# Optimization experiments

Measured on AMD Instinct MI355X. Metric: run time of the kernel, lower is better.

## Reference

```python
import jax, jax.numpy as jnp
import numpy as np

NUM_HEADS = 16

def setup_inputs() -> dict:
    key = jax.random.key(0)
    ks = jax.random.split(key, 5)
    b, n, d = 2, 2048, 1024
    s = 0.02
    return {
        "x": jax.random.normal(ks[0], (b, n, d), jnp.float32),
        "wq": jax.random.normal(ks[1], (d, d), jnp.float32) * s,
        "wk": jax.random.normal(ks[2], (d, d), jnp.float32) * s,
        "wv": jax.random.normal(ks[3], (d, d), jnp.float32) * s,
        "wo": jax.random.normal(ks[4], (d, d), jnp.float32) * s,
        "bo": jnp.zeros((d,), jnp.float32),
    }

def reference(x, wq, wk, wv, wo, bo):
    b, n, c = x.shape
    h = NUM_HEADS
    hd = c // h
    scale = hd ** -0.5
    # qkv projections (qkv_bias=False); torch Linear computes x @ W.T
    def split_heads(t):
        return t.reshape(b, n, h, hd).transpose(0, 2, 1, 3)  # b h n d
    q = split_heads(x @ wq.T)
    k = split_heads(x @ wk.T)
    v = split_heads(x @ wv.T)
    dots = jnp.einsum('bhid,bhjd->bhij', q, k) * scale
    attn = jax.nn.softmax(dots, axis=-1)  # attn_drop=0 -> identity
    out = jnp.einsum('bhij,bhjd->bhid', attn, v)
    out = out.transpose(0, 2, 1, 3).reshape(b, n, c)
    out = out @ wo.T + bo  # proj_drop=0 -> identity
    return out
```

## Files before the change

kernel.cpp:

```cpp
#include <hip/hip_runtime.h>
#include <hip/hip_bf16.h>

typedef float f32x4 __attribute__((ext_vector_type(4)));
typedef short short8 __attribute__((ext_vector_type(8)));
typedef short short4v __attribute__((ext_vector_type(4)));

#define MFMA(a, b, c) __builtin_amdgcn_mfma_f32_16x16x32_bf16((a), (b), (c), 0, 0, 0)

#if __has_builtin(__builtin_amdgcn_exp2f)
#define EXP2(x) __builtin_amdgcn_exp2f(x)
#else
#define EXP2(x) exp2f(x)
#endif

#define B_  2
#define N_  2048
#define C_  1024
#define H_  16
#define HD_ 64
#define M_  (B_ * N_)

#define QSCALE 0.18033688011112042f

typedef const __attribute__((address_space(1))) void* gp_t;
typedef __attribute__((address_space(3))) void* sp_t;
#define GLL16(g, s) __builtin_amdgcn_global_load_lds((gp_t)(const void*)(g), (sp_t)(void*)(s), 16, 0, 0)

__device__ __forceinline__ short f2bf(float f) {
    union { float fv; unsigned u; } v; v.fv = f;
    unsigned r = v.u + 0x7fffu + ((v.u >> 16) & 1u);
    return (short)(r >> 16);
}
__device__ __forceinline__ unsigned pack_rne(float a, float b) {
    return (unsigned)(unsigned short)f2bf(a) | ((unsigned)(unsigned short)f2bf(b) << 16);
}

__global__ __launch_bounds__(256) void convert_kernel(
    const float* __restrict__ x,  const float* __restrict__ wq,
    const float* __restrict__ wk, const float* __restrict__ wv,
    const float* __restrict__ wo, short* __restrict__ dst)
{
    size_t e = ((size_t)blockIdx.x * 256 + threadIdx.x) * 8;
    const float* src; size_t off;
    if (e < 4194304)      { src = x;  off = e; }
    else if (e < 5242880) { src = wq; off = e - 4194304; }
    else if (e < 6291456) { src = wk; off = e - 5242880; }
    else if (e < 7340032) { src = wv; off = e - 6291456; }
    else                  { src = wo; off = e - 7340032; }
    float4 a = *(const float4*)(src + off);
    float4 b = *(const float4*)(src + off + 4);
    short8 s;
    s[0] = f2bf(a.x); s[1] = f2bf(a.y); s[2] = f2bf(a.z); s[3] = f2bf(a.w);
    s[4] = f2bf(b.x); s[5] = f2bf(b.y); s[6] = f2bf(b.z); s[7] = f2bf(b.w);
    *(short8*)(dst + e) = s;
}

__global__ __launch_bounds__(256) void qkv_gemm(
    const short* __restrict__ xb, const short* __restrict__ Wb,
    short* __restrict__ Qb, short* __restrict__ Kb, short* __restrict__ Vt)
{
    const int m0 = blockIdx.x * 128;
    const int n0 = blockIdx.y * 128;
    __shared__ short As[128 * 32];
    __shared__ short Bs[128 * 32];
    const int tid  = threadIdx.x;
    const int wave = tid >> 6, lane = tid & 63;
    const int quad = lane >> 4, l16 = lane & 15;
    const int wr = (wave >> 1) * 64, wc = (wave & 1) * 64;

    f32x4 acc[4][4] = {};

    for (int kk = 0; kk < C_; kk += 32) {
        __syncthreads();
        #pragma unroll
        for (int it = 0; it < 2; ++it) {
            int f = (it * 256 + tid) * 8;
            int row = f >> 5, col = f & 31;
            GLL16(xb + (size_t)(m0 + row) * C_ + kk + col, &As[f]);
            GLL16(Wb + (size_t)(n0 + row) * C_ + kk + col, &Bs[f]);
        }
        __syncthreads();
        short8 af[4], bf[4];
        #pragma unroll
        for (int mi = 0; mi < 4; ++mi) af[mi] = *(const short8*)&As[(wr + mi * 16 + l16) * 32 + quad * 8];
        #pragma unroll
        for (int ni = 0; ni < 4; ++ni) bf[ni] = *(const short8*)&Bs[(wc + ni * 16 + l16) * 32 + quad * 8];
        #pragma unroll
        for (int mi = 0; mi < 4; ++mi)
        #pragma unroll
        for (int ni = 0; ni < 4; ++ni)
            acc[mi][ni] = MFMA(af[mi], bf[ni], acc[mi][ni]);
    }

    const int which = n0 >> 10;
    const int nb = n0 & 1023;
    #pragma unroll
    for (int mi = 0; mi < 4; ++mi)
    #pragma unroll
    for (int ni = 0; ni < 4; ++ni)
    #pragma unroll
    for (int r = 0; r < 4; ++r) {
        int m  = m0 + wr + mi * 16 + quad * 4 + r;
        int cc = nb + wc + ni * 16 + l16;
        float av = acc[mi][ni][r];
        if (which == 0) av *= QSCALE;
        short bv = f2bf(av);
        int bb = m >> 11, ns = m & (N_ - 1);
        int h = cc >> 6, d = cc & 63;
        size_t bh = (size_t)(bb * H_ + h);
        if (which == 0)      Qb[(bh * N_ + ns) * HD_ + d] = bv;
        else if (which == 1) Kb[(bh * N_ + ns) * HD_ + d] = bv;
        else                 Vt[(bh * HD_ + d) * N_ + ns] = bv;
    }
}

__global__ __launch_bounds__(256, 2) void attn_kernel(
    const short* __restrict__ Qb, const short* __restrict__ Kb,
    const short* __restrict__ Vt, short* __restrict__ Ob)
{
    const int bh = blockIdx.y;
    const int b = bh >> 4, h = bh & (H_ - 1);
    const int i0 = blockIdx.x * 128;
    __shared__ short Qs[128 * 64];
    __shared__ short Ks[2][64 * 64];
    __shared__ short Vs[2][64 * 64];
    const int tid  = threadIdx.x;
    const int wave = tid >> 6, lane = tid & 63;
    const int quad = lane >> 4, l16 = lane & 15;
    const int sw = l16 & 7;

    const short* Qg = Qb + ((size_t)bh * N_ + i0) * HD_;
    const short* Kg = Kb + (size_t)bh * N_ * HD_;
    const short* Vg = Vt + (size_t)bh * HD_ * N_;

    const int row0 = tid >> 3,  c0 = (tid & 7) ^ (row0 & 7);
    const int row1 = row0 + 32, c1 = (tid & 7) ^ (row1 & 7);
    const short* KgA0 = Kg + row0 * HD_ + c0 * 8;
    const short* KgA1 = Kg + row1 * HD_ + c1 * 8;
    const short* VgA0 = Vg + (size_t)row0 * N_ + c0 * 8;
    const short* VgA1 = Vg + (size_t)row1 * N_ + c1 * 8;

    #pragma unroll
    for (int it = 0; it < 4; ++it) {
        int s = it * 256 + tid;
        int row = s >> 3, c = (s & 7) ^ (row & 7);
        GLL16(Qg + row * HD_ + c * 8, &Qs[s * 8]);
    }
    GLL16(KgA0, &Ks[0][tid * 8]);
    GLL16(KgA1, &Ks[0][(tid + 256) * 8]);
    GLL16(VgA0, &Vs[0][tid * 8]);
    GLL16(VgA1, &Vs[0][(tid + 256) * 8]);
    __syncthreads();

    short8 qf[2][2];
    #pragma unroll
    for (int s = 0; s < 2; ++s) {
        int row = (wave * 32 + s * 16 + l16) * 64;
        qf[s][0] = *(const short8*)&Qs[row + ((quad ^ sw) * 8)];
        qf[s][1] = *(const short8*)&Qs[row + (((quad + 4) ^ sw) * 8)];
    }

    f32x4 o[2][4] = {};
    float lrow[2] = {0.f, 0.f};

    for (int jt = 0; jt < N_ / 64; ++jt) {
        const int cur = jt & 1;
        if (jt + 1 < N_ / 64) {
            int j1 = (jt + 1) * 64;
            GLL16(KgA0 + (size_t)j1 * HD_, &Ks[cur ^ 1][tid * 8]);
            GLL16(KgA1 + (size_t)j1 * HD_, &Ks[cur ^ 1][(tid + 256) * 8]);
            GLL16(VgA0 + j1, &Vs[cur ^ 1][tid * 8]);
            GLL16(VgA1 + j1, &Vs[cur ^ 1][(tid + 256) * 8]);
        }
        const short* Kc = Ks[cur];
        const short* Vc = Vs[cur];

        #pragma unroll
        for (int half = 0; half < 2; ++half) {
            unsigned pq[2][4];
            #pragma unroll
            for (int nio = 0; nio < 2; ++nio) {
                int ni = half * 2 + nio;
                int krow = (ni * 16 + l16) * 64;
                short8 kf0 = *(const short8*)&Kc[krow + ((quad ^ sw) * 8)];
                short8 kf1 = *(const short8*)&Kc[krow + (((quad + 4) ^ sw) * 8)];
                #pragma unroll
                for (int s = 0; s < 2; ++s) {
                    f32x4 st = {0.f, 0.f, 0.f, 0.f};
                    st = MFMA(kf0, qf[s][0], st);
                    st = MFMA(kf1, qf[s][1], st);
                    union { float f; unsigned u; } e0, e1, e2, e3;
                    e0.f = EXP2(st[0]); e1.f = EXP2(st[1]);
                    e2.f = EXP2(st[2]); e3.f = EXP2(st[3]);
                    lrow[s] += (e0.f + e1.f) + (e2.f + e3.f);
                    pq[s][nio * 2]     = (e0.u >> 16) | (e1.u & 0xffff0000u);
                    pq[s][nio * 2 + 1] = (e2.u >> 16) | (e3.u & 0xffff0000u);
                }
            }
            #pragma unroll
            for (int di = 0; di < 4; ++di) {
                int vrow = (di * 16 + l16) * 64;
                int ch1 = (half * 4 +     (quad >> 1)) ^ sw;
                int ch2 = (half * 4 + 2 + (quad >> 1)) ^ sw;
                union { struct { short4v lo, hi; } p; short8 v; } va;
                va.p.lo = *(const short4v*)&Vc[vrow + ch1 * 8 + (quad & 1) * 4];
                va.p.hi = *(const short4v*)&Vc[vrow + ch2 * 8 + (quad & 1) * 4];
                #pragma unroll
                for (int s = 0; s < 2; ++s) {
                    union { unsigned u[4]; short8 v; } pb;
                    pb.u[0] = pq[s][0]; pb.u[1] = pq[s][1];
                    pb.u[2] = pq[s][2]; pb.u[3] = pq[s][3];
                    o[s][di] = MFMA(va.v, pb.v, o[s][di]);
                }
            }
        }
        __syncthreads();
    }

    #pragma unroll
    for (int s = 0; s < 2; ++s) {
        float l = lrow[s];
        l += __shfl_xor(l, 16, 64);
        l += __shfl_xor(l, 32, 64);
        float inv = 1.f / l;
        int ig = i0 + wave * 32 + s * 16 + l16;
        size_t base = ((size_t)(b * N_ + ig)) * C_ + h * HD_;
        #pragma unroll
        for (int di = 0; di < 4; ++di) {
            unsigned p01 = pack_rne(o[s][di][0] * inv, o[s][di][1] * inv);
            unsigned p23 = pack_rne(o[s][di][2] * inv, o[s][di][3] * inv);
            *(unsigned*)&Ob[base + di * 16 + quad * 4]     = p01;
            *(unsigned*)&Ob[base + di * 16 + quad * 4 + 2] = p23;
        }
    }
}

__global__ __launch_bounds__(256) void proj_gemm(
    const short* __restrict__ Ob, const short* __restrict__ wob,
    const float* __restrict__ bo, float* __restrict__ out)
{
    const int m0 = blockIdx.x * 64;
    const int n0 = blockIdx.y * 128;
    __shared__ short As[64 * 32];
    __shared__ short Bs[128 * 32];
    const int tid  = threadIdx.x;
    const int wave = tid >> 6, lane = tid & 63;
    const int quad = lane >> 4, l16 = lane & 15;
    const int wr = (wave >> 1) * 32, wc = (wave & 1) * 64;

    f32x4 acc[2][4] = {};

    for (int kk = 0; kk < C_; kk += 32) {
        __syncthreads();
        {
            int f = tid * 8;
            int row = f >> 5, col = f & 31;
            GLL16(Ob + (size_t)(m0 + row) * C_ + kk + col, &As[f]);
        }
        #pragma unroll
        for (int it = 0; it < 2; ++it) {
            int f = (it * 256 + tid) * 8;
            int row = f >> 5, col = f & 31;
            GLL16(wob + (size_t)(n0 + row) * C_ + kk + col, &Bs[f]);
        }
        __syncthreads();
        short8 af[2], bf[4];
        #pragma unroll
        for (int mi = 0; mi < 2; ++mi) af[mi] = *(const short8*)&As[(wr + mi * 16 + l16) * 32 + quad * 8];
        #pragma unroll
        for (int ni = 0; ni < 4; ++ni) bf[ni] = *(const short8*)&Bs[(wc + ni * 16 + l16) * 32 + quad * 8];
        #pragma unroll
        for (int mi = 0; mi < 2; ++mi)
        #pragma unroll
        for (int ni = 0; ni < 4; ++ni)
            acc[mi][ni] = MFMA(af[mi], bf[ni], acc[mi][ni]);
    }

    #pragma unroll
    for (int mi = 0; mi < 2; ++mi)
    #pragma unroll
    for (int ni = 0; ni < 4; ++ni)
    #pragma unroll
    for (int r = 0; r < 4; ++r) {
        int m = m0 + wr + mi * 16 + quad * 4 + r;
        int c = n0 + wc + ni * 16 + l16;
        out[(size_t)m * C_ + c] = acc[mi][ni][r] + bo[c];
    }
}

extern "C" void kernel_launch(void* const* d_in, const int* in_sizes, int n_in,
                              void* d_out, int out_size, void* d_ws, size_t ws_size,
                              hipStream_t stream) {
    const float* x  = (const float*)d_in[0];
    const float* wq = (const float*)d_in[1];
    const float* wk = (const float*)d_in[2];
    const float* wv = (const float*)d_in[3];
    const float* wo = (const float*)d_in[4];
    const float* bo = (const float*)d_in[5];
    float* out = (float*)d_out;

    short* xb  = (short*)d_ws;
    short* Wb  = xb  + 4194304;
    short* wob = Wb  + 3145728;
    short* Qb  = wob + 1048576;
    short* Kb  = Qb  + 4194304;
    short* Vt  = Kb  + 4194304;
    short* Obuf= Vt  + 4194304;

    dim3 blk(256);
    convert_kernel<<<4096, blk, 0, stream>>>(x, wq, wk, wv, wo, xb);
    qkv_gemm<<<dim3(M_ / 128, 3072 / 128), blk, 0, stream>>>(xb, Wb, Qb, Kb, Vt);
    attn_kernel<<<dim3(N_ / 128, B_ * H_), blk, 0, stream>>>(Qb, Kb, Vt, Obuf);
    proj_gemm<<<dim3(M_ / 64, C_ / 128), blk, 0, stream>>>(Obuf, wob, bo, out);
}
```

Before: 191.8 us.

## Triple-buffer QKV GEMM loads with swizzled LDS, block swizzle, and MFMA priority hints

Restructures the QKV projection GEMM into a three-stage LDS ring, issuing global-to-LDS loads two tiles ahead and replacing the double __syncthreads with one vmcnt wait plus a barrier per step. It XOR-swizzles the LDS layout to cut bank conflicts, remaps block indices for better L2 reuse, and adds setprio around MFMA groups in both the GEMM and the attention kernel. The extra LDS and the occupancy hint may limit waves per CU.

```diff
diff --git a/kernel.cpp b/kernel.cpp
--- a/kernel.cpp
+++ b/kernel.cpp
@@ -55,42 +55,75 @@
     *(short8*)(dst + e) = s;
 }
 
-__global__ __launch_bounds__(256) void qkv_gemm(
+__global__ __launch_bounds__(256, 3) void qkv_gemm(
     const short* __restrict__ xb, const short* __restrict__ Wb,
     short* __restrict__ Qb, short* __restrict__ Kb, short* __restrict__ Vt)
 {
-    const int m0 = blockIdx.x * 128;
-    const int n0 = blockIdx.y * 128;
-    __shared__ short As[128 * 32];
-    __shared__ short Bs[128 * 32];
+    __shared__ short As[3][128 * 32];
+    __shared__ short Bs[3][128 * 32];
     const int tid  = threadIdx.x;
     const int wave = tid >> 6, lane = tid & 63;
     const int quad = lane >> 4, l16 = lane & 15;
     const int wr = (wave >> 1) * 64, wc = (wave & 1) * 64;
 
+    const int bid = blockIdx.y * 32 + blockIdx.x;
+    const int swz = (bid & 7) * 96 + (bid >> 3);
+    const int m0 = (swz & 31) * 128;
+    const int n0 = (swz >> 5) * 128;
+
+    const int s0 = tid, s1 = tid + 256;
+    const int r0 = s0 >> 2, g0 = (s0 & 3) ^ (((r0 >> 1) ^ (r0 >> 3)) & 3);
+    const int r1 = s1 >> 2, g1 = (s1 & 3) ^ (((r1 >> 1) ^ (r1 >> 3)) & 3);
+    const short* A0 = xb + (size_t)(m0 + r0) * C_ + g0 * 8;
+    const short* A1 = xb + (size_t)(m0 + r1) * C_ + g1 * 8;
+    const short* B0 = Wb + (size_t)(n0 + r0) * C_ + g0 * 8;
+    const short* B1 = Wb + (size_t)(n0 + r1) * C_ + g1 * 8;
+
+#define QKV_STAGE(slot, kk) do { \
+    GLL16(A0 + (kk), &As[slot][tid * 8]); \
+    GLL16(A1 + (kk), &As[slot][(tid + 256) * 8]); \
+    GLL16(B0 + (kk), &Bs[slot][tid * 8]); \
+    GLL16(B1 + (kk), &Bs[slot][(tid + 256) * 8]); } while (0)
+
+    QKV_STAGE(0, 0);
+    QKV_STAGE(1, 32);
+    asm volatile("s_waitcnt vmcnt(4)" ::: "memory");
+    __builtin_amdgcn_s_barrier();
+    __builtin_amdgcn_sched_barrier(0);
+
+    const int baseA = wr + l16, baseB = wc + l16;
+    const int pA = (quad ^ (((baseA >> 1) ^ (baseA >> 3)) & 3)) << 3;
+    const int pB = (quad ^ (((baseB >> 1) ^ (baseB >> 3)) & 3)) << 3;
+
     f32x4 acc[4][4] = {};
-
-    for (int kk = 0; kk < C_; kk += 32) {
-        __syncthreads();
-        #pragma unroll
-        for (int it = 0; it < 2; ++it) {
-            int f = (it * 256 + tid) * 8;
-            int row = f >> 5, col = f & 31;
-            GLL16(xb + (size_t)(m0 + row) * C_ + kk + col, &As[f]);
-            GLL16(Wb + (size_t)(n0 + row) * C_ + kk + col, &Bs[f]);
-        }
-        __syncthreads();
+    int cur = 0, nslot = 2;
+    for (int t = 0; t < 32; ++t) {
+        if (t + 2 < 32) QKV_STAGE(nslot, (t + 2) * 32);
         short8 af[4], bf[4];
         #pragma unroll
-        for (int mi = 0; mi < 4; ++mi) af[mi] = *(const short8*)&As[(wr + mi * 16 + l16) * 32 + quad * 8];
-        #pragma unroll
-        for (int ni = 0; ni < 4; ++ni) bf[ni] = *(const short8*)&Bs[(wc + ni * 16 + l16) * 32 + quad * 8];
+        for (int mi = 0; mi < 4; ++mi)
+            af[mi] = *(const short8*)&As[cur][(baseA + mi * 16) * 32 + (pA ^ ((mi & 1) << 4))];
+        #pragma unroll
+        for (int ni = 0; ni < 4; ++ni)
+            bf[ni] = *(const short8*)&Bs[cur][(baseB + ni * 16) * 32 + (pB ^ ((ni & 1) << 4))];
+        __builtin_amdgcn_s_setprio(1);
         #pragma unroll
         for (int mi = 0; mi < 4; ++mi)
         #pragma unroll
         for (int ni = 0; ni < 4; ++ni)
             acc[mi][ni] = MFMA(af[mi], bf[ni], acc[mi][ni]);
-    }
+        __builtin_amdgcn_s_setprio(0);
+        if (t + 1 < 32) {
+            __builtin_amdgcn_sched_barrier(0);
+            if (t + 2 < 32) asm volatile("s_waitcnt vmcnt(4)" ::: "memory");
+            else            asm volatile("s_waitcnt vmcnt(0)" ::: "memory");
+            __builtin_amdgcn_s_barrier();
+            __builtin_amdgcn_sched_barrier(0);
+        }
+        cur   = (cur   == 2) ? 0 : cur + 1;
+        nslot = (nslot == 2) ? 0 : nslot + 1;
+    }
+#undef QKV_STAGE
 
     const int which = n0 >> 10;
     const int nb = n0 & 1023;
@@ -187,8 +220,10 @@
                 #pragma unroll
                 for (int s = 0; s < 2; ++s) {
                     f32x4 st = {0.f, 0.f, 0.f, 0.f};
+                    __builtin_amdgcn_s_setprio(1);
                     st = MFMA(kf0, qf[s][0], st);
                     st = MFMA(kf1, qf[s][1], st);
+                    __builtin_amdgcn_s_setprio(0);
                     union { float f; unsigned u; } e0, e1, e2, e3;
                     e0.f = EXP2(st[0]); e1.f = EXP2(st[1]);
                     e2.f = EXP2(st[2]); e3.f = EXP2(st[3]);
@@ -205,6 +240,7 @@
                 union { struct { short4v lo, hi; } p; short8 v; } va;
                 va.p.lo = *(const short4v*)&Vc[vrow + ch1 * 8 + (quad & 1) * 4];
                 va.p.hi = *(const short4v*)&Vc[vrow + ch2 * 8 + (quad & 1) * 4];
+                __builtin_amdgcn_s_setprio(1);
                 #pragma unroll
                 for (int s = 0; s < 2; ++s) {
                     union { unsigned u[4]; short8 v; } pb;
@@ -212,6 +248,7 @@
                     pb.u[2] = pq[s][2]; pb.u[3] = pq[s][3];
                     o[s][di] = MFMA(va.v, pb.v, o[s][di]);
                 }
+                __builtin_amdgcn_s_setprio(0);
             }
         }
         __syncthreads();
```

Result: slower. 204.7 us (+6.7%).

## Shrink attention query tile to 64 rows, raise occupancy, swizzle blocks, prioritize MFMA

Applied to the files above, without the earlier changes.

Each attention block now handles 64 query rows instead of 128, with each wave owning 16 rows. This halves per-wave accumulator registers and doubles the grid to 1024 blocks, and launch bounds move to 4 blocks per SM so more waves can hide latency. Block IDs are swizzled so that consecutive blocks spread across different heads. s_setprio is placed around the MFMAs to favour matrix issue. The cost is that K/V tiles are reloaded twice as often relative to the compute done on them.

```diff
diff --git a/kernel.cpp b/kernel.cpp
--- a/kernel.cpp
+++ b/kernel.cpp
@@ -114,14 +114,16 @@
     }
 }
 
-__global__ __launch_bounds__(256, 2) void attn_kernel(
+__global__ __launch_bounds__(256, 4) void attn_kernel(
     const short* __restrict__ Qb, const short* __restrict__ Kb,
     const short* __restrict__ Vt, short* __restrict__ Ob)
 {
-    const int bh = blockIdx.y;
+    const int bid = blockIdx.y * 32 + blockIdx.x;
+    const int swz = (bid & 7) * 128 + (bid >> 3);
+    const int bh = swz >> 5;
+    const int i0 = (swz & 31) * 64;
     const int b = bh >> 4, h = bh & (H_ - 1);
-    const int i0 = blockIdx.x * 128;
-    __shared__ short Qs[128 * 64];
+    __shared__ short Qs[64 * 64];
     __shared__ short Ks[2][64 * 64];
     __shared__ short Vs[2][64 * 64];
     const int tid  = threadIdx.x;
@@ -141,7 +143,7 @@
     const short* VgA1 = Vg + (size_t)row1 * N_ + c1 * 8;
 
     #pragma unroll
-    for (int it = 0; it < 4; ++it) {
+    for (int it = 0; it < 2; ++it) {
         int s = it * 256 + tid;
         int row = s >> 3, c = (s & 7) ^ (row & 7);
         GLL16(Qg + row * HD_ + c * 8, &Qs[s * 8]);
@@ -152,16 +154,15 @@
     GLL16(VgA1, &Vs[0][(tid + 256) * 8]);
     __syncthreads();
 
-    short8 qf[2][2];
-    #pragma unroll
-    for (int s = 0; s < 2; ++s) {
-        int row = (wave * 32 + s * 16 + l16) * 64;
-        qf[s][0] = *(const short8*)&Qs[row + ((quad ^ sw) * 8)];
-        qf[s][1] = *(const short8*)&Qs[row + (((quad + 4) ^ sw) * 8)];
-    }
-
-    f32x4 o[2][4] = {};
-    float lrow[2] = {0.f, 0.f};
+    short8 qf[2];
+    {
+        int row = (wave * 16 + l16) * 64;
+        qf[0] = *(const short8*)&Qs[row + ((quad ^ sw) * 8)];
+        qf[1] = *(const short8*)&Qs[row + (((quad + 4) ^ sw) * 8)];
+    }
+
+    f32x4 o[4] = {};
+    float lrow = 0.f;
 
     for (int jt = 0; jt < N_ / 64; ++jt) {
         const int cur = jt & 1;
@@ -177,25 +178,24 @@
 
         #pragma unroll
         for (int half = 0; half < 2; ++half) {
-            unsigned pq[2][4];
+            unsigned pq[4];
             #pragma unroll
             for (int nio = 0; nio < 2; ++nio) {
                 int ni = half * 2 + nio;
                 int krow = (ni * 16 + l16) * 64;
                 short8 kf0 = *(const short8*)&Kc[krow + ((quad ^ sw) * 8)];
                 short8 kf1 = *(const short8*)&Kc[krow + (((quad + 4) ^ sw) * 8)];
-                #pragma unroll
-                for (int s = 0; s < 2; ++s) {
-                    f32x4 st = {0.f, 0.f, 0.f, 0.f};
-                    st = MFMA(kf0, qf[s][0], st);
-                    st = MFMA(kf1, qf[s][1], st);
-                    union { float f; unsigned u; } e0, e1, e2, e3;
-                    e0.f = EXP2(st[0]); e1.f = EXP2(st[1]);
-                    e2.f = EXP2(st[2]); e3.f = EXP2(st[3]);
-                    lrow[s] += (e0.f + e1.f) + (e2.f + e3.f);
-                    pq[s][nio * 2]     = (e0.u >> 16) | (e1.u & 0xffff0000u);
-                    pq[s][nio * 2 + 1] = (e2.u >> 16) | (e3.u & 0xffff0000u);
-                }
+                f32x4 st = {0.f, 0.f, 0.f, 0.f};
+                __builtin_amdgcn_s_setprio(1);
+                st = MFMA(kf0, qf[0], st);
+                st = MFMA(kf1, qf[1], st);
+                __builtin_amdgcn_s_setprio(0);
+                union { float f; unsigned u; } e0, e1, e2, e3;
+                e0.f = EXP2(st[0]); e1.f = EXP2(st[1]);
+                e2.f = EXP2(st[2]); e3.f = EXP2(st[3]);
+                lrow += (e0.f + e1.f) + (e2.f + e3.f);
+                pq[nio * 2]     = (e0.u >> 16) | (e1.u & 0xffff0000u);
+                pq[nio * 2 + 1] = (e2.u >> 16) | (e3.u & 0xffff0000u);
             }
             #pragma unroll
             for (int di = 0; di < 4; ++di) {
@@ -205,30 +205,28 @@
                 union { struct { short4v lo, hi; } p; short8 v; } va;
                 va.p.lo = *(const short4v*)&Vc[vrow + ch1 * 8 + (quad & 1) * 4];
                 va.p.hi = *(const short4v*)&Vc[vrow + ch2 * 8 + (quad & 1) * 4];
-                #pragma unroll
-                for (int s = 0; s < 2; ++s) {
-                    union { unsigned u[4]; short8 v; } pb;
-                    pb.u[0] = pq[s][0]; pb.u[1] = pq[s][1];
-                    pb.u[2] = pq[s][2]; pb.u[3] = pq[s][3];
-                    o[s][di] = MFMA(va.v, pb.v, o[s][di]);
-                }
+                union { unsigned u[4]; short8 v; } pb;
+                pb.u[0] = pq[0]; pb.u[1] = pq[1];
+                pb.u[2] = pq[2]; pb.u[3] = pq[3];
+                __builtin_amdgcn_s_setprio(1);
+                o[di] = MFMA(va.v, pb.v, o[di]);
+                __builtin_amdgcn_s_setprio(0);
             }
         }
         __syncthreads();
     }
 
-    #pragma unroll
-    for (int s = 0; s < 2; ++s) {
-        float l = lrow[s];
+    {
+        float l = lrow;
         l += __shfl_xor(l, 16, 64);
         l += __shfl_xor(l, 32, 64);
         float inv = 1.f / l;
-        int ig = i0 + wave * 32 + s * 16 + l16;
+        int ig = i0 + wave * 16 + l16;
         size_t base = ((size_t)(b * N_ + ig)) * C_ + h * HD_;
         #pragma unroll
         for (int di = 0; di < 4; ++di) {
-            unsigned p01 = pack_rne(o[s][di][0] * inv, o[s][di][1] * inv);
-            unsigned p23 = pack_rne(o[s][di][2] * inv, o[s][di][3] * inv);
+            unsigned p01 = pack_rne(o[di][0] * inv, o[di][1] * inv);
+            unsigned p23 = pack_rne(o[di][2] * inv, o[di][3] * inv);
             *(unsigned*)&Ob[base + di * 16 + quad * 4]     = p01;
             *(unsigned*)&Ob[base + di * 16 + quad * 4 + 2] = p23;
         }
@@ -310,6 +308,6 @@
     dim3 blk(256);
     convert_kernel<<<4096, blk, 0, stream>>>(x, wq, wk, wv, wo, xb);
     qkv_gemm<<<dim3(M_ / 128, 3072 / 128), blk, 0, stream>>>(xb, Wb, Qb, Kb, Vt);
-    attn_kernel<<<dim3(N_ / 128, B_ * H_), blk, 0, stream>>>(Qb, Kb, Vt, Obuf);
+    attn_kernel<<<dim3(N_ / 64, B_ * H_), blk, 0, stream>>>(Qb, Kb, Vt, Obuf);
     proj_gemm<<<dim3(M_ / 64, C_ / 128), blk, 0, stream>>>(Obuf, wob, bo, out);
 }
```

After: 188.5 us. Within noise of the previous version (-1.8%).
